# Kernel tuning notes

Measured on AMD Instinct MI355X. Metric: run time of the kernel, lower is better.

Reference implementation:

```python
import jax, jax.numpy as jnp
import numpy as np

N_VERTS, N_RADIAL, N_ANGULAR, FEAT = 100000, 5, 8, 16
AMT_TEMPLATES, OUTPUT_DIM = 8, 32


def setup_inputs() -> dict:
    key = jax.random.key(0)
    k1, k2, k3, k4, k5, k6 = jax.random.split(key, 6)
    mesh_signal = jax.random.normal(k1, (N_VERTS, FEAT), dtype=jnp.float32)
    bary_weights = jax.random.uniform(k2, (N_VERTS, N_RADIAL, N_ANGULAR, 3), dtype=jnp.float32)
    interp_coeffs = jax.random.uniform(
        k3, (N_RADIAL, N_ANGULAR, N_RADIAL * N_ANGULAR), dtype=jnp.float32)
    template_weights = jax.random.normal(
        k4, (AMT_TEMPLATES, OUTPUT_DIM, FEAT), dtype=jnp.float32)
    bias = jax.random.normal(k5, (AMT_TEMPLATES, OUTPUT_DIM), dtype=jnp.float32)
    bary_indices = jax.random.randint(k6, (N_VERTS, N_RADIAL, N_ANGULAR, 3), 0, N_VERTS, dtype=jnp.int32)
    return {
        "mesh_signal": mesh_signal,
        "bary_weights": bary_weights,
        "interp_coeffs": interp_coeffs,
        "template_weights": template_weights,
        "bias": bias,
        "bary_indices": bary_indices,
    }


def reference(mesh_signal, bary_weights, interp_coeffs, template_weights, bias, bary_indices):
    n, R, A, _ = bary_indices.shape
    K = R * A
    # --- patch operator: barycentric gather + weighted interpolation ---
    gathered = mesh_signal[bary_indices]                         # (n, R, A, 3, F)
    interp = jnp.einsum('nrak,nrakf->nraf', bary_weights, gathered)  # (n, R, A, F)
    # --- prior: matvec with interpolation coefficients over flattened template ---
    flat = interp.reshape(n, K, -1)                              # (n, K, F)
    interp = jnp.einsum('nkf,rak->nraf', flat, interp_coeffs)    # (n, R, A, F)
    # --- fold: W @ X then reduce_sum over template-vertex axis. Since the
    # activation comes AFTER the reduce_sum, sum(W @ X, -1) == W @ sum(X, -1),
    # so we reduce first to avoid an (n, T, O, K) intermediate. ---
    s = interp.reshape(n, K, -1).sum(axis=1)                     # (n, F)
    pre = jnp.einsum('tof,nf->nto', template_weights, s) + bias  # (n, T, O)
    act = jax.nn.relu(pre)
    return act.sum(axis=1)                                       # (n, O)
```

## Files before the change

### kernel.cpp

```cpp
#include <hip/hip_runtime.h>

#define KK 40
#define M3 120
#define MM4 30
#define RCH 15
#define FEAT 16
#define NT 8
#define ODIM 32
#define VPB 32
#define BLOCK 256
#define SST 17

typedef unsigned int u32;
typedef unsigned short u16;
typedef float  f32x4 __attribute__((ext_vector_type(4)));
typedef int    i32x4 __attribute__((ext_vector_type(4)));
typedef u32    u32x4 __attribute__((ext_vector_type(4)));

__global__ void cs3_kernel(const float* __restrict__ ic, float* __restrict__ cs3) {
    __shared__ float cs[KK];
    const int t = threadIdx.x;
    if (t < KK) {
        float s = 0.f;
        #pragma unroll
        for (int ra = 0; ra < KK; ++ra) s += ic[ra * KK + t];
        cs[t] = s;
    }
    __syncthreads();
    if (t < M3) cs3[t] = cs[t / 3];
}

__device__ __forceinline__ u16 f2bf_rne(float x) {
    u32 u = __float_as_uint(x);
    u32 r = (u + 0x7fffu + ((u >> 16) & 1u)) >> 16;
    return (u16)r;
}

__global__ void cvt_kernel(const float* __restrict__ mesh, u16* __restrict__ mbf, int total) {
    const int i = blockIdx.x * blockDim.x + threadIdx.x;
    const int base = i * 8;
    if (base < total) {
        f32x4 a = __builtin_nontemporal_load((const f32x4*)(mesh + base));
        f32x4 b = __builtin_nontemporal_load((const f32x4*)(mesh + base + 4));
        u32x4 v;
        v.x = (u32)f2bf_rne(a.x) | ((u32)f2bf_rne(a.y) << 16);
        v.y = (u32)f2bf_rne(a.z) | ((u32)f2bf_rne(a.w) << 16);
        v.z = (u32)f2bf_rne(b.x) | ((u32)f2bf_rne(b.y) << 16);
        v.w = (u32)f2bf_rne(b.z) | ((u32)f2bf_rne(b.w) << 16);
        __builtin_nontemporal_store(v, (u32x4*)(mbf + base));
    }
}

__global__ __launch_bounds__(BLOCK, 8) void conv_kernel(
    const u16*   __restrict__ mbf,
    const float* __restrict__ bw,
    const float* __restrict__ W,
    const float* __restrict__ bias,
    const int*   __restrict__ bi,
    const float* __restrict__ cs3,
    float*       __restrict__ out,
    int n)
{
    __shared__ f32x4 s_buf[VPB * SST * 2];
    __shared__ float s_sig[VPB][FEAT + 1];

    f32x4* s_bw4 = s_buf;
    i32x4* s_bi4 = (i32x4*)(s_buf + VPB * SST);
    float (*s_out)[ODIM + 1] = (float(*)[ODIM + 1])s_buf;

    const int tid = threadIdx.x;
    const int vg0 = blockIdx.x * VPB;

    const f32x4* bw4g  = (const f32x4*)bw;
    const i32x4* bi4g  = (const i32x4*)bi;
    const f32x4* cs34g = (const f32x4*)cs3;

    const int vloc = tid >> 3;
    const int jc   = (tid >> 2) & 1;
    const int mc   = (tid >> 1) & 1;
    const int q    = tid & 1;
    const int vg   = vg0 + vloc;

    float acc[8];
    #pragma unroll
    for (int e = 0; e < 8; ++e) acc[e] = 0.f;

    #pragma unroll
    for (int r = 0; r < 2; ++r) {
        if (r) __syncthreads();

        #pragma unroll
        for (int ii = 0; ii < 2; ++ii) {
            const int i = tid + ii * BLOCK;
            if (i < VPB * RCH) {
                const int v = i / RCH;
                const int c = i - v * RCH;
                if (vg0 + v < n) {
                    const int gchunk = (vg0 + v) * MM4 + r * RCH + c;
                    f32x4 wv = __builtin_nontemporal_load(bw4g + gchunk);
                    i32x4 iv = __builtin_nontemporal_load(bi4g + gchunk);
                    const f32x4 cc = cs34g[r * RCH + c];
                    wv.x *= cc.x; wv.y *= cc.y; wv.z *= cc.z; wv.w *= cc.w;
                    s_bw4[v * SST + c] = wv;
                    s_bi4[v * SST + c] = iv;
                }
            }
        }
        __syncthreads();

        if (vg < n) {
            #pragma unroll
            for (int i = 0; i < 8; ++i) {
                const int c = mc + 2 * i;
                if (c < RCH) {
                    const f32x4 wc = s_bw4[vloc * SST + c];
                    const i32x4 iv = s_bi4[vloc * SST + c];
                    const float w0 = jc ? wc.z : wc.x;
                    const float w1 = jc ? wc.w : wc.y;
                    const int   i0 = jc ? iv.z : iv.x;
                    const int   i1 = jc ? iv.w : iv.y;

                    const u32x4 g0 = *((const u32x4*)(mbf + (size_t)i0 * FEAT) + q);
                    const u32x4 g1 = *((const u32x4*)(mbf + (size_t)i1 * FEAT) + q);

                    acc[0] = fmaf(w0, __uint_as_float(g0.x << 16),          acc[0]);
                    acc[1] = fmaf(w0, __uint_as_float(g0.x & 0xffff0000u), acc[1]);
                    acc[2] = fmaf(w0, __uint_as_float(g0.y << 16),          acc[2]);
                    acc[3] = fmaf(w0, __uint_as_float(g0.y & 0xffff0000u), acc[3]);
                    acc[4] = fmaf(w0, __uint_as_float(g0.z << 16),          acc[4]);
                    acc[5] = fmaf(w0, __uint_as_float(g0.z & 0xffff0000u), acc[5]);
                    acc[6] = fmaf(w0, __uint_as_float(g0.w << 16),          acc[6]);
                    acc[7] = fmaf(w0, __uint_as_float(g0.w & 0xffff0000u), acc[7]);

                    acc[0] = fmaf(w1, __uint_as_float(g1.x << 16),          acc[0]);
                    acc[1] = fmaf(w1, __uint_as_float(g1.x & 0xffff0000u), acc[1]);
                    acc[2] = fmaf(w1, __uint_as_float(g1.y << 16),          acc[2]);
                    acc[3] = fmaf(w1, __uint_as_float(g1.y & 0xffff0000u), acc[3]);
                    acc[4] = fmaf(w1, __uint_as_float(g1.z << 16),          acc[4]);
                    acc[5] = fmaf(w1, __uint_as_float(g1.z & 0xffff0000u), acc[5]);
                    acc[6] = fmaf(w1, __uint_as_float(g1.w << 16),          acc[6]);
                    acc[7] = fmaf(w1, __uint_as_float(g1.w & 0xffff0000u), acc[7]);
                }
            }
        }
    }

    #pragma unroll
    for (int e = 0; e < 8; ++e) acc[e] += __shfl_xor(acc[e], 4);
    #pragma unroll
    for (int e = 0; e < 8; ++e) acc[e] += __shfl_xor(acc[e], 2);

    if (jc == 0) {
        const f32x4 v = (mc == 0) ? (f32x4){acc[0], acc[1], acc[2], acc[3]}
                                  : (f32x4){acc[4], acc[5], acc[6], acc[7]};
        *(f32x4*)(&s_sig[vloc][q * 8 + mc * 4]) = v;
    }
    __syncthreads();

    {
        const int lane = tid & 63;
        const int wave = __builtin_amdgcn_readfirstlane(tid >> 6);
        const int v    = lane & (VPB - 1);

        float s[FEAT];
        #pragma unroll
        for (int f = 0; f < FEAT; ++f) s[f] = s_sig[v][f];

        float oacc[8];
        #pragma unroll
        for (int oi = 0; oi < 8; ++oi) oacc[oi] = 0.f;

        #pragma unroll 2
        for (int t = 0; t < NT; ++t) {
            #pragma unroll
            for (int oi = 0; oi < 8; ++oi) {
                const int o = wave * 8 + oi;
                float pre = bias[t * ODIM + o];
                const float* wrow = W + ((size_t)t * ODIM + o) * FEAT;
                #pragma unroll
                for (int f = 0; f < FEAT; ++f)
                    pre = fmaf(wrow[f], s[f], pre);
                oacc[oi] += fmaxf(pre, 0.f);
            }
        }

        if (lane < VPB) {
            #pragma unroll
            for (int oi = 0; oi < 8; ++oi)
                s_out[v][wave * 8 + oi] = oacc[oi];
        }
    }
    __syncthreads();

    {
        const int v  = tid >> 3;
        const int oq = tid & 7;
        const int vgo = vg0 + v;
        if (vgo < n) {
            const f32x4 val = { s_out[v][oq * 4 + 0], s_out[v][oq * 4 + 1],
                                s_out[v][oq * 4 + 2], s_out[v][oq * 4 + 3] };
            __builtin_nontemporal_store(val, (f32x4*)(out + (size_t)vgo * ODIM + oq * 4));
        }
    }
}

extern "C" void kernel_launch(void* const* d_in, const int* in_sizes, int n_in,
                              void* d_out, int out_size, void* d_ws, size_t ws_size,
                              hipStream_t stream) {
    const float* mesh = (const float*)d_in[0];
    const float* bw   = (const float*)d_in[1];
    const float* ic   = (const float*)d_in[2];
    const float* W    = (const float*)d_in[3];
    const float* bias = (const float*)d_in[4];
    const int*   bi   = (const int*)d_in[5];
    float* out = (float*)d_out;

    const int n = in_sizes[0] / FEAT;
    const int total = n * FEAT;

    float* cs3 = (float*)d_ws;
    u16*   mbf = (u16*)((char*)d_ws + 512);

    cs3_kernel<<<1, 128, 0, stream>>>(ic, cs3);

    const int cvt_threads = (total + 7) / 8;
    cvt_kernel<<<(cvt_threads + 255) / 256, 256, 0, stream>>>(mesh, mbf, total);

    const int blocks = (n + VPB - 1) / VPB;
    conv_kernel<<<blocks, BLOCK, 0, stream>>>(mbf, bw, W, bias, bi, cs3, out, n);
}
```

Before: 104.3 us.

## Double vertices per block, use packed FMA, and stop duplicate lane work in MLP

Raises the block to 64 vertices and 512 threads so that all 64 lanes of each wave handle a distinct vertex in the template/ReLU stage; before, lanes 32-63 repeated the work of lanes 0-31. Each wave now computes 4 outputs instead of 8. The gather accumulation uses float2 elementwise FMA, which can map to packed FP32 FMA, and walks contiguous chunk pairs per thread so more gathers are in flight. In exchange, launch bounds of 512 threads with 8 blocks may squeeze the register budget. The 16-byte LDS store into 33-float rows may also be misaligned.

```diff
diff --git a/kernel.cpp b/kernel.cpp
--- a/kernel.cpp
+++ b/kernel.cpp
@@ -7,12 +7,13 @@
 #define FEAT 16
 #define NT 8
 #define ODIM 32
-#define VPB 32
-#define BLOCK 256
+#define VPB 64
+#define BLOCK 512
 #define SST 17
 
 typedef unsigned int u32;
 typedef unsigned short u16;
+typedef float  f32x2 __attribute__((ext_vector_type(2)));
 typedef float  f32x4 __attribute__((ext_vector_type(4)));
 typedef int    i32x4 __attribute__((ext_vector_type(4)));
 typedef u32    u32x4 __attribute__((ext_vector_type(4)));
@@ -51,6 +52,23 @@
     }
 }
 
+__device__ __forceinline__ void acc8(f32x2 acc2[4], const u32x4 g, const float s) {
+    const f32x2 s2 = {s, s};
+    f32x2 p;
+    p.x = __uint_as_float(g.x << 16);
+    p.y = __uint_as_float(g.x & 0xffff0000u);
+    acc2[0] = __builtin_elementwise_fma(p, s2, acc2[0]);
+    p.x = __uint_as_float(g.y << 16);
+    p.y = __uint_as_float(g.y & 0xffff0000u);
+    acc2[1] = __builtin_elementwise_fma(p, s2, acc2[1]);
+    p.x = __uint_as_float(g.z << 16);
+    p.y = __uint_as_float(g.z & 0xffff0000u);
+    acc2[2] = __builtin_elementwise_fma(p, s2, acc2[2]);
+    p.x = __uint_as_float(g.w << 16);
+    p.y = __uint_as_float(g.w & 0xffff0000u);
+    acc2[3] = __builtin_elementwise_fma(p, s2, acc2[3]);
+}
+
 __global__ __launch_bounds__(BLOCK, 8) void conv_kernel(
     const u16*   __restrict__ mbf,
     const float* __restrict__ bw,
@@ -81,9 +99,9 @@
     const int q    = tid & 1;
     const int vg   = vg0 + vloc;
 
-    float acc[8];
-    #pragma unroll
-    for (int e = 0; e < 8; ++e) acc[e] = 0.f;
+    f32x2 acc2[4];
+    #pragma unroll
+    for (int e = 0; e < 4; ++e) acc2[e] = (f32x2){0.f, 0.f};
 
     #pragma unroll
     for (int r = 0; r < 2; ++r) {
@@ -109,50 +127,53 @@
         __syncthreads();
 
         if (vg < n) {
+            const int cbase = mc ? 8 : 0;
             #pragma unroll
-            for (int i = 0; i < 8; ++i) {
-                const int c = mc + 2 * i;
-                if (c < RCH) {
-                    const f32x4 wc = s_bw4[vloc * SST + c];
-                    const i32x4 iv = s_bi4[vloc * SST + c];
-                    const float w0 = jc ? wc.z : wc.x;
-                    const float w1 = jc ? wc.w : wc.y;
-                    const int   i0 = jc ? iv.z : iv.x;
-                    const int   i1 = jc ? iv.w : iv.y;
-
-                    const u32x4 g0 = *((const u32x4*)(mbf + (size_t)i0 * FEAT) + q);
-                    const u32x4 g1 = *((const u32x4*)(mbf + (size_t)i1 * FEAT) + q);
-
-                    acc[0] = fmaf(w0, __uint_as_float(g0.x << 16),          acc[0]);
-                    acc[1] = fmaf(w0, __uint_as_float(g0.x & 0xffff0000u), acc[1]);
-                    acc[2] = fmaf(w0, __uint_as_float(g0.y << 16),          acc[2]);
-                    acc[3] = fmaf(w0, __uint_as_float(g0.y & 0xffff0000u), acc[3]);
-                    acc[4] = fmaf(w0, __uint_as_float(g0.z << 16),          acc[4]);
-                    acc[5] = fmaf(w0, __uint_as_float(g0.z & 0xffff0000u), acc[5]);
-                    acc[6] = fmaf(w0, __uint_as_float(g0.w << 16),          acc[6]);
-                    acc[7] = fmaf(w0, __uint_as_float(g0.w & 0xffff0000u), acc[7]);
-
-                    acc[0] = fmaf(w1, __uint_as_float(g1.x << 16),          acc[0]);
-                    acc[1] = fmaf(w1, __uint_as_float(g1.x & 0xffff0000u), acc[1]);
-                    acc[2] = fmaf(w1, __uint_as_float(g1.y << 16),          acc[2]);
-                    acc[3] = fmaf(w1, __uint_as_float(g1.y & 0xffff0000u), acc[3]);
-                    acc[4] = fmaf(w1, __uint_as_float(g1.z << 16),          acc[4]);
-                    acc[5] = fmaf(w1, __uint_as_float(g1.z & 0xffff0000u), acc[5]);
-                    acc[6] = fmaf(w1, __uint_as_float(g1.w << 16),          acc[6]);
-                    acc[7] = fmaf(w1, __uint_as_float(g1.w & 0xffff0000u), acc[7]);
+            for (int ib = 0; ib < 4; ++ib) {
+                const int c0 = cbase + 2 * ib;
+                const int c1 = c0 + 1;
+                const bool has1 = !(mc && (ib == 3));
+
+                const f32x4 wA = s_bw4[vloc * SST + c0];
+                const i32x4 iA = s_bi4[vloc * SST + c0];
+                const float wa0 = jc ? wA.z : wA.x;
+                const float wa1 = jc ? wA.w : wA.y;
+                const int   ia0 = jc ? iA.z : iA.x;
+                const int   ia1 = jc ? iA.w : iA.y;
+                const u32x4 gA0 = *((const u32x4*)(mbf + (size_t)ia0 * FEAT) + q);
+                const u32x4 gA1 = *((const u32x4*)(mbf + (size_t)ia1 * FEAT) + q);
+
+                if (has1) {
+                    const f32x4 wB = s_bw4[vloc * SST + c1];
+                    const i32x4 iB = s_bi4[vloc * SST + c1];
+                    const float wb0 = jc ? wB.z : wB.x;
+                    const float wb1 = jc ? wB.w : wB.y;
+                    const int   ib0 = jc ? iB.z : iB.x;
+                    const int   ib1 = jc ? iB.w : iB.y;
+                    const u32x4 gB0 = *((const u32x4*)(mbf + (size_t)ib0 * FEAT) + q);
+                    const u32x4 gB1 = *((const u32x4*)(mbf + (size_t)ib1 * FEAT) + q);
+                    acc8(acc2, gA0, wa0);
+                    acc8(acc2, gA1, wa1);
+                    acc8(acc2, gB0, wb0);
+                    acc8(acc2, gB1, wb1);
+                } else {
+                    acc8(acc2, gA0, wa0);
+                    acc8(acc2, gA1, wa1);
                 }
             }
         }
     }
 
-    #pragma unroll
-    for (int e = 0; e < 8; ++e) acc[e] += __shfl_xor(acc[e], 4);
-    #pragma unroll
-    for (int e = 0; e < 8; ++e) acc[e] += __shfl_xor(acc[e], 2);
+    float a8[8] = { acc2[0].x, acc2[0].y, acc2[1].x, acc2[1].y,
+                    acc2[2].x, acc2[2].y, acc2[3].x, acc2[3].y };
+    #pragma unroll
+    for (int e = 0; e < 8; ++e) a8[e] += __shfl_xor(a8[e], 4);
+    #pragma unroll
+    for (int e = 0; e < 8; ++e) a8[e] += __shfl_xor(a8[e], 2);
 
     if (jc == 0) {
-        const f32x4 v = (mc == 0) ? (f32x4){acc[0], acc[1], acc[2], acc[3]}
-                                  : (f32x4){acc[4], acc[5], acc[6], acc[7]};
+        const f32x4 v = (mc == 0) ? (f32x4){a8[0], a8[1], a8[2], a8[3]}
+                                  : (f32x4){a8[4], a8[5], a8[6], a8[7]};
         *(f32x4*)(&s_sig[vloc][q * 8 + mc * 4]) = v;
     }
     __syncthreads();
@@ -160,21 +181,20 @@
     {
         const int lane = tid & 63;
         const int wave = __builtin_amdgcn_readfirstlane(tid >> 6);
-        const int v    = lane & (VPB - 1);
 
         float s[FEAT];
         #pragma unroll
-        for (int f = 0; f < FEAT; ++f) s[f] = s_sig[v][f];
-
-        float oacc[8];
-        #pragma unroll
-        for (int oi = 0; oi < 8; ++oi) oacc[oi] = 0.f;
+        for (int f = 0; f < FEAT; ++f) s[f] = s_sig[lane][f];
+
+        float oacc[4];
+        #pragma unroll
+        for (int oi = 0; oi < 4; ++oi) oacc[oi] = 0.f;
 
         #pragma unroll 2
         for (int t = 0; t < NT; ++t) {
             #pragma unroll
-            for (int oi = 0; oi < 8; ++oi) {
-                const int o = wave * 8 + oi;
+            for (int oi = 0; oi < 4; ++oi) {
+                const int o = wave * 4 + oi;
                 float pre = bias[t * ODIM + o];
                 const float* wrow = W + ((size_t)t * ODIM + o) * FEAT;
                 #pragma unroll
@@ -184,17 +204,13 @@
             }
         }
 
-        if (lane < VPB) {
-            #pragma unroll
-            for (int oi = 0; oi < 8; ++oi)
-                s_out[v][wave * 8 + oi] = oacc[oi];
-        }
+        *(f32x4*)(&s_out[lane][wave * 4]) = (f32x4){oacc[0], oacc[1], oacc[2], oacc[3]};
     }
     __syncthreads();
 
     {
-        const int v  = tid >> 3;
-        const int oq = tid & 7;
+        const int v   = tid >> 3;
+        const int oq  = tid & 7;
         const int vgo = vg0 + v;
         if (vgo < n) {
             const f32x4 val = { s_out[v][oq * 4 + 0], s_out[v][oq * 4 + 1],
```

Result: slower. 108.7 us (+4.2%).
